# Kernel tuning notes

Measured on AMD Instinct MI355X. Metric: run time of the kernel, lower is better.

Reference implementation:

```python
import jax, jax.numpy as jnp
import numpy as np

H = 16  # n_heads (init kwarg)


def pos_enc(length, dim):
    # torch PositionalEncoding: pe[:,0::2]=sin, pe[:,1::2]=cos
    pos = jnp.arange(length, dtype=jnp.float32)[:, None]
    div = jnp.exp(jnp.arange(0, dim, 2, dtype=jnp.float32) * (-np.log(10000.0) / dim))
    ang = pos * div  # [L, dim/2]
    return jnp.stack([jnp.sin(ang), jnp.cos(ang)], axis=-1).reshape(length, dim)


def torch_ln(x, a, b, eps=1e-6):
    # custom LayerNorm: a*(x-mean)/(std+eps)+b with unbiased std (torch default)
    mean = x.mean(-1, keepdims=True)
    n = x.shape[-1]
    var = ((x - mean) ** 2).sum(-1, keepdims=True) / (n - 1)
    return a * (x - mean) / (jnp.sqrt(var) + eps) + b


def setup_inputs() -> dict:
    key = jax.random.key(0)
    ks = jax.random.split(key, 16)
    B, Lq, Lk, qd, kd, hid, mid = 8, 512, 1024, 768, 768, 1024, 4096
    s = 0.02  # weight init scale
    w = lambda k, shape: jax.random.normal(k, shape, jnp.float32) * s
    return dict(
        q=jax.random.normal(ks[0], (B, Lq, qd), jnp.float32),
        k=jax.random.normal(ks[1], (B, Lk, kd), jnp.float32),
        Wq=w(ks[2], (qd, hid)), bq=jnp.zeros(hid, jnp.float32),
        Wk=w(ks[3], (kd, hid)), bk=jnp.zeros(hid, jnp.float32),
        Wv=w(ks[4], (kd, hid)), bv=jnp.zeros(hid, jnp.float32),
        Wv0=w(ks[5], (kd, hid)), bv0=jnp.zeros(hid, jnp.float32),
        Wq0=w(ks[6], (qd, hid)), bq0=jnp.zeros(hid, jnp.float32),
        nq_a=jnp.ones(hid, jnp.float32), nq_b=jnp.zeros(hid, jnp.float32),
        nx_a=jnp.ones(hid, jnp.float32), nx_b=jnp.zeros(hid, jnp.float32),
        W1=w(ks[7], (hid, mid)), b1=jnp.zeros(mid, jnp.float32),
        W2=w(ks[8], (mid, hid)), b2=jnp.zeros(hid, jnp.float32),
        ns_a=jnp.ones(hid, jnp.float32), ns_b=jnp.zeros(hid, jnp.float32),
    )


def reference(q, k, Wq, bq, Wk, bk, Wv, bv, Wv0, bv0, Wq0, bq0,
              nq_a, nq_b, nx_a, nx_b, W1, b1, W2, b2, ns_a, ns_b):
    # FocalAtt(mode='CA').forward(q, k, PE='qk', SF=True, outmode='atted_bilinear')
    B, Lq, qd = q.shape
    Lk, kd = k.shape[1], k.shape[2]
    hid = Wq.shape[1]
    dh = hid // H
    q0 = q
    qp = q + pos_enc(Lq, qd)  # PosEnc_q (dropout=0)
    kp = k + pos_enc(Lk, kd)  # PosEnc_k
    # AttM: manual multi-head scores
    qh = (qp @ Wq + bq).reshape(B, Lq, H, dh).transpose(0, 2, 1, 3)  # bhqd
    kh = (kp @ Wk + bk).reshape(B, Lk, H, dh).transpose(0, 2, 1, 3)  # bhkd
    scores = jnp.einsum('bhqd,bhkd->bhqk', qh, kh) / jnp.sqrt(jnp.float32(dh))
    att = jax.nn.softmax(scores, axis=-1)  # SF=True
    q0p = q0 @ Wq0 + bq0  # [B, Lq, hid]
    # 'atted' branch
    v1 = (kp @ Wv + bv).reshape(B, Lk, H, dh).transpose(0, 2, 1, 3)
    atted = jnp.einsum('bhqk,bhkd->bhqd', att, v1)
    atted = atted.transpose(0, 2, 1, 3).reshape(B, Lq, hid)
    atted = torch_ln(q0p + atted, nq_a, nq_b)
    # 'bilinear' branch: einsum('bhvk,bhvq,bhqk->bhk')
    q0h = q0p.reshape(B, Lq, H, dh).transpose(0, 2, 1, 3)  # bhvd, v=Lq
    v0 = (kp @ Wv0 + bv0).reshape(B, Lk, H, dh).transpose(0, 2, 1, 3)  # bhqd, q=Lk
    x = jnp.einsum('bhvd,bhvq,bhqd->bhd', q0h, att, v0).reshape(B, hid)
    x = torch_ln(x, nx_a, nx_b)
    # attention output: relu over scores, mean over heads
    att_out = jax.nn.relu(scores).sum(axis=1) / jnp.float32(H)  # [B, Lq, Lk]
    # SorCA: FFN + residual + LayerNorm
    ff = jax.nn.relu(atted @ W1 + b1) @ W2 + b2
    qq = torch_ln(atted + ff, ns_a, ns_b)
    # FocalAtt returns (feature, q, k, attention, attidx_q, attidx_k); drop Nones
    return (x, qq, kp, att_out)
```

## Files before the change

kernel.cpp:

```cpp
#include <hip/hip_runtime.h>


typedef unsigned short bfr;
using short8 = __attribute__((ext_vector_type(8))) short;
using f32x4  = __attribute__((ext_vector_type(4))) float;

__device__ __forceinline__ float b2f(bfr s) {
  return __uint_as_float(((unsigned int)s) << 16);
}
__device__ __forceinline__ bfr f2b(float f) {
  unsigned int u = __float_as_uint(f);
  u += 0x7fffu + ((u >> 16) & 1u);
  return (bfr)(u >> 16);
}

struct __align__(8) us4 { bfr x, y, z, w; };

__device__ __forceinline__ float4 load4f(const float* p) { return *(const float4*)p; }
__device__ __forceinline__ float4 load4f(const bfr* p) {
  us4 u = *(const us4*)p;
  return make_float4(b2f(u.x), b2f(u.y), b2f(u.z), b2f(u.w));
}
__device__ __forceinline__ void store4(float* p, float a, float b, float c, float d) {
  *(float4*)p = make_float4(a, b, c, d);
}
__device__ __forceinline__ void store4(bfr* p, float a, float b, float c, float d) {
  us4 v; v.x = f2b(a); v.y = f2b(b); v.z = f2b(c); v.w = f2b(d);
  *(us4*)p = v;
}

__device__ __forceinline__ void gll16(const bfr* g, bfr* l) {
  __builtin_amdgcn_global_load_lds(
      (const __attribute__((address_space(1))) unsigned int*)g,
      (__attribute__((address_space(3))) unsigned int*)l, 16, 0, 0);
}

__device__ __forceinline__ int swz_off(int row, int chunk) {
  return row * 64 + ((chunk ^ (row & 7)) * 8);
}

__device__ __forceinline__ float pe_val(int l, int d) {
  float ang = (float)l * expf((float)(d & ~1) * (-9.210340371976184f / 768.0f));
  return (d & 1) ? cosf(ang) : sinf(ang);
}

__global__ __launch_bounds__(256) void posenc_k(const float* __restrict__ in,
                                                float* __restrict__ outf,
                                                bfr* __restrict__ outb, int total) {
  int idx = blockIdx.x * 256 + threadIdx.x;
  if (idx >= total) return;
  float v = in[idx] + pe_val((idx / 768) % 1024, idx % 768);
  outf[idx] = v;
  outb[idx] = f2b(v);
}

__global__ __launch_bounds__(256) void posenc_q_all(const float* __restrict__ in,
                                                    bfr* __restrict__ out,
                                                    bfr* __restrict__ outraw,
                                                    int total) {
  int idx = blockIdx.x * 256 + threadIdx.x;
  if (idx >= total) return;
  float v = in[idx];
  out[idx] = f2b(v + pe_val((idx / 768) % 512, idx % 768));
  outraw[idx] = f2b(v);
}

__global__ __launch_bounds__(256) void transpose_w(const float* __restrict__ src,
                                                   bfr* __restrict__ dst,
                                                   int rows, int cols, int ld,
                                                   int mode) {
  __shared__ float t[32][33];
  const int bc = blockIdx.x * 32, br = blockIdx.y * 32;
  const int tx = threadIdx.x & 31, ty = threadIdx.x >> 5;
#pragma unroll
  for (int i = 0; i < 4; i++)
    t[ty + i * 8][tx] = src[(size_t)(br + ty + i * 8) * ld + bc + tx];
  __syncthreads();
#pragma unroll
  for (int i = 0; i < 4; i++) {
    int c = bc + ty + i * 8;
    int r = (mode == 0) ? c : ((c >> 6) * 128 + (c & 63) + (mode == 2 ? 64 : 0));
    dst[(size_t)r * rows + br + tx] = f2b(t[tx][ty + i * 8]);
  }
}

template <typename TC>
__device__ __forceinline__ void mgemm_body64(const bfr* __restrict__ A,
                                             const bfr* __restrict__ BT,
                                             const float* __restrict__ bias,
                                             TC* __restrict__ C,
                                             int K, int ldc, int relu, int accum,
                                             int m0, int n0,
                                             bfr* __restrict__ As,
                                             bfr* __restrict__ Bs) {
  const int tid = threadIdx.x;
  const int lane = tid & 63, w = tid >> 6;
  const int wm = (w & 1) * 64, wn = (w >> 1) * 32;
  const int grow = lane >> 3;
  const int gkc = ((lane & 7) ^ (lane >> 3)) * 8;
  const int fr = lane & 15, fcg = lane >> 4;
  const int NT = K >> 6;
  f32x4 acc[4][2];
#pragma unroll
  for (int i = 0; i < 4; i++)
#pragma unroll
    for (int j = 0; j < 2; j++) acc[i][j] = (f32x4){0.f, 0.f, 0.f, 0.f};

  auto issue = [&](int t, int buf) {
    const int k0 = t << 6;
    const bfr* Ag = A + (size_t)(m0 + w * 32 + grow) * K + k0 + gkc;
#pragma unroll
    for (int i = 0; i < 4; i++)
      gll16(Ag + (size_t)(i * 8) * K, As + buf * 8192 + (w * 32 + i * 8) * 64);
    const bfr* Bg = BT + (size_t)(n0 + w * 16 + grow) * K + k0 + gkc;
#pragma unroll
    for (int i = 0; i < 2; i++)
      gll16(Bg + (size_t)(i * 8) * K, Bs + buf * 4096 + (w * 16 + i * 8) * 64);
  };

  issue(0, 0);
  issue(1, 1);
  asm volatile("s_waitcnt vmcnt(6)" ::: "memory");
  __builtin_amdgcn_s_barrier();
  __builtin_amdgcn_sched_barrier(0);
  int cur = 0, ib = 2;
  for (int t = 0; t < NT; ++t) {
    if (t + 2 < NT) {
      issue(t + 2, ib);
      ib = (ib == 2) ? 0 : ib + 1;
    }
    __builtin_amdgcn_s_setprio(1);
#pragma unroll
    for (int ks = 0; ks < 2; ks++) {
      short8 af[4], bf4[2];
#pragma unroll
      for (int i = 0; i < 4; i++)
        af[i] = *(const short8*)(As + cur * 8192 + swz_off(wm + i * 16 + fr, ks * 4 + fcg));
#pragma unroll
      for (int j = 0; j < 2; j++)
        bf4[j] = *(const short8*)(Bs + cur * 4096 + swz_off(wn + j * 16 + fr, ks * 4 + fcg));
#pragma unroll
      for (int i = 0; i < 4; i++)
#pragma unroll
        for (int j = 0; j < 2; j++)
          acc[i][j] = __builtin_amdgcn_mfma_f32_16x16x32_bf16(af[i], bf4[j], acc[i][j], 0, 0, 0);
    }
    __builtin_amdgcn_s_setprio(0);
    if (t + 1 < NT) {
      if (t + 2 < NT)
        asm volatile("s_waitcnt vmcnt(6)" ::: "memory");
      else
        asm volatile("s_waitcnt vmcnt(0)" ::: "memory");
      __builtin_amdgcn_s_barrier();
      __builtin_amdgcn_sched_barrier(0);
      cur = (cur == 2) ? 0 : cur + 1;
    }
  }
  const int col0 = n0 + wn + fr;
  const int row0 = m0 + wm + (lane >> 4) * 4;
  float bsv[2];
#pragma unroll
  for (int j = 0; j < 2; j++) bsv[j] = bias ? bias[col0 + j * 16] : 0.f;
#pragma unroll
  for (int i = 0; i < 4; i++) {
#pragma unroll
    for (int j = 0; j < 2; j++) {
      const int col = col0 + j * 16;
#pragma unroll
      for (int r = 0; r < 4; r++) {
        const int row = row0 + i * 16 + r;
        float v = acc[i][j][r] + bsv[j];
        if (relu) v = fmaxf(v, 0.f);
        size_t idx = (size_t)row * ldc + col;
        if constexpr (sizeof(TC) == 2) {
          C[idx] = f2b(v);
        } else {
          if (accum) C[idx] += v; else C[idx] = v;
        }
      }
    }
  }
}

template <typename TC>
__global__ __launch_bounds__(256) void mgemm64(const bfr* __restrict__ A,
                                               const bfr* __restrict__ BT,
                                               const float* __restrict__ bias,
                                               TC* __restrict__ C,
                                               int K, int ldc, int relu, int accum) {
  __shared__ bfr As[3][8192];
  __shared__ bfr Bs[3][4096];
  const int nwg = gridDim.x * gridDim.y;
  const int bid = blockIdx.y * gridDim.x + blockIdx.x;
  const int q8 = nwg >> 3, r8 = nwg & 7;
  const int xcd = bid & 7, off = bid >> 3;
  const int swz = (xcd < r8 ? xcd * (q8 + 1) : r8 * (q8 + 1) + (xcd - r8) * q8) + off;
  const int n0 = (swz % gridDim.x) * 64, m0 = (swz / gridDim.x) * 128;
  mgemm_body64<TC>(A, BT, bias, C, K, ldc, relu, accum, m0, n0,
                   &As[0][0], &Bs[0][0]);
}

__global__ __launch_bounds__(256) void kv_gemm2(const bfr* __restrict__ kp0,
                                                const bfr* __restrict__ kp1,
                                                const bfr* __restrict__ WkT,
                                                const float* __restrict__ bk,
                                                bfr* __restrict__ kh0,
                                                bfr* __restrict__ kh1,
                                                const bfr* __restrict__ WTvv,
                                                bfr* __restrict__ vT0,
                                                bfr* __restrict__ vT1) {
  __shared__ bfr As[3][8192];
  __shared__ bfr Bs[3][4096];
  const int swz = (blockIdx.x & 7) * 96 + (blockIdx.x >> 3);
  if (swz < 128) {
    mgemm_body64<bfr>(kp0, WkT, bk, kh0, 768, 1024, 0, 0,
                      (swz >> 4) * 128, (swz & 15) * 64, &As[0][0], &Bs[0][0]);
  } else if (swz < 256) {
    const int s = swz - 128;
    mgemm_body64<bfr>(kp1, WkT, bk, kh1, 768, 1024, 0, 0,
                      (s >> 4) * 128, (s & 15) * 64, &As[0][0], &Bs[0][0]);
  } else if (swz < 512) {
    const int s = swz - 256;
    mgemm_body64<bfr>(WTvv, kp0, nullptr, vT0, 768, 1024, 0, 0,
                      (s >> 4) * 128, (s & 15) * 64, &As[0][0], &Bs[0][0]);
  } else {
    const int s = swz - 512;
    mgemm_body64<bfr>(WTvv, kp1, nullptr, vT1, 768, 1024, 0, 0,
                      (s >> 4) * 128, (s & 15) * 64, &As[0][0], &Bs[0][0]);
  }
}

__global__ __launch_bounds__(256) void proj_gemm(const bfr* __restrict__ q16,
                                                 const bfr* __restrict__ Wq0T,
                                                 const float* __restrict__ bq0,
                                                 bfr* __restrict__ q0p,
                                                 const bfr* __restrict__ qp_all,
                                                 const bfr* __restrict__ WqT,
                                                 const float* __restrict__ bq,
                                                 bfr* __restrict__ qh) {
  __shared__ bfr As[3][8192];
  __shared__ bfr Bs[3][4096];
  const int swz = (blockIdx.x & 7) * 128 + (blockIdx.x >> 3);
  if (swz < 512) {
    mgemm_body64<bfr>(q16, Wq0T, bq0, q0p, 768, 1024, 0, 0,
                      (swz >> 4) * 128, (swz & 15) * 64, &As[0][0], &Bs[0][0]);
  } else {
    const int s = swz - 512;
    mgemm_body64<bfr>(qp_all, WqT, bq, qh, 768, 1024, 0, 0,
                      (s >> 4) * 128, (s & 15) * 64, &As[0][0], &Bs[0][0]);
  }
}

__global__ __launch_bounds__(256) void score_mfma(const bfr* __restrict__ qh,
                                                  const bfr* __restrict__ kh,
                                                  bfr* __restrict__ sc) {
  __shared__ __align__(16) bfr Qs[128][72];
  __shared__ __align__(16) bfr Ks[128][72];
  const int h = blockIdx.z, q0 = blockIdx.y * 128, k0 = blockIdx.x * 128;
  const int tid = threadIdx.x, lane = tid & 63;
  const int wm = ((tid >> 6) & 1) * 64, wn = (tid >> 7) * 64;
  const int fr = lane & 15, fc = (lane >> 4) * 8;
  {
    const int r = tid >> 1, c = (tid & 1) * 32;
    const bfr* qsrc = qh + (size_t)(q0 + r) * 1024 + h * 64 + c;
    const bfr* ksrc = kh + (size_t)(k0 + r) * 1024 + h * 64 + c;
#pragma unroll
    for (int i = 0; i < 4; i++) {
      *(short8*)&Qs[r][c + i * 8] = *(const short8*)(qsrc + i * 8);
      *(short8*)&Ks[r][c + i * 8] = *(const short8*)(ksrc + i * 8);
    }
  }
  __syncthreads();
  f32x4 acc[4][4];
#pragma unroll
  for (int i = 0; i < 4; i++)
#pragma unroll
    for (int j = 0; j < 4; j++) acc[i][j] = (f32x4){0.f, 0.f, 0.f, 0.f};
  __builtin_amdgcn_s_setprio(1);
#pragma unroll
  for (int ks = 0; ks < 2; ks++) {
    short8 af[4], bf[4];
#pragma unroll
    for (int t = 0; t < 4; t++) af[t] = *(const short8*)&Qs[wm + t * 16 + fr][ks * 32 + fc];
#pragma unroll
    for (int t = 0; t < 4; t++) bf[t] = *(const short8*)&Ks[wn + t * 16 + fr][ks * 32 + fc];
#pragma unroll
    for (int i = 0; i < 4; i++)
#pragma unroll
      for (int j = 0; j < 4; j++)
        acc[i][j] = __builtin_amdgcn_mfma_f32_16x16x32_bf16(af[i], bf[j], acc[i][j], 0, 0, 0);
  }
  __builtin_amdgcn_s_setprio(0);
  const int col0 = k0 + wn + fr;
  const int row0 = q0 + wm + (lane >> 4) * 4;
#pragma unroll
  for (int i = 0; i < 4; i++)
#pragma unroll
    for (int j = 0; j < 4; j++)
#pragma unroll
      for (int r = 0; r < 4; r++)
        sc[((size_t)h * 512 + row0 + i * 16 + r) * 1024 + col0 + j * 16] =
            f2b(acc[i][j][r] * 0.125f);
}

__global__ __launch_bounds__(256) void smax_ao(bfr* __restrict__ sc,
                                               float* __restrict__ ao) {
  __shared__ float part[4][1024];
  const int q = blockIdx.x;
  const int tid = threadIdx.x, lane = tid & 63, w = tid >> 6;
  float aos[16];
#pragma unroll
  for (int i = 0; i < 16; i++) aos[i] = 0.f;
#pragma unroll
  for (int i = 0; i < 4; i++) {
    const int h = w * 4 + i;
    bfr* row = sc + ((size_t)h * 512 + q) * 1024 + lane * 16;
    us4 raw[4];
    float v[16];
#pragma unroll
    for (int j = 0; j < 4; j++) raw[j] = ((const us4*)row)[j];
#pragma unroll
    for (int j = 0; j < 4; j++) {
      v[j * 4 + 0] = b2f(raw[j].x); v[j * 4 + 1] = b2f(raw[j].y);
      v[j * 4 + 2] = b2f(raw[j].z); v[j * 4 + 3] = b2f(raw[j].w);
    }
    float m = v[0];
#pragma unroll
    for (int j = 1; j < 16; j++) m = fmaxf(m, v[j]);
#pragma unroll
    for (int j = 0; j < 16; j++) aos[j] += fmaxf(v[j], 0.f);
    for (int o = 32; o; o >>= 1) m = fmaxf(m, __shfl_xor(m, o, 64));
    float s = 0.f;
#pragma unroll
    for (int j = 0; j < 16; j++) { v[j] = expf(v[j] - m); s += v[j]; }
    for (int o = 32; o; o >>= 1) s += __shfl_xor(s, o, 64);
    const float inv = 1.0f / s;
#pragma unroll
    for (int j = 0; j < 4; j++) {
      raw[j].x = f2b(v[j * 4 + 0] * inv); raw[j].y = f2b(v[j * 4 + 1] * inv);
      raw[j].z = f2b(v[j * 4 + 2] * inv); raw[j].w = f2b(v[j * 4 + 3] * inv);
      ((us4*)row)[j] = raw[j];
    }
  }
#pragma unroll
  for (int j = 0; j < 4; j++)
    *(float4*)&part[w][lane * 16 + j * 4] =
        make_float4(aos[j * 4], aos[j * 4 + 1], aos[j * 4 + 2], aos[j * 4 + 3]);
  __syncthreads();
  const int k4 = tid * 4;
  float4 a0 = *(const float4*)&part[0][k4];
  float4 a1 = *(const float4*)&part[1][k4];
  float4 a2 = *(const float4*)&part[2][k4];
  float4 a3 = *(const float4*)&part[3][k4];
  store4(ao + (size_t)q * 1024 + k4,
         (a0.x + a1.x + a2.x + a3.x) * 0.0625f, (a0.y + a1.y + a2.y + a3.y) * 0.0625f,
         (a0.z + a1.z + a2.z + a3.z) * 0.0625f, (a0.w + a1.w + a2.w + a3.w) * 0.0625f);
}

__global__ __launch_bounds__(256) void attv2(const bfr* __restrict__ att,
                                             const bfr* __restrict__ vT,
                                             const float* __restrict__ bv,
                                             const float* __restrict__ bv0,
                                             bfr* __restrict__ atp,
                                             bfr* __restrict__ u) {
  __shared__ bfr As[3][32 * 64];
  __shared__ bfr Bs[3][128 * 64];
  const int h = blockIdx.y, q0 = blockIdx.x * 32;
  const int tid = threadIdx.x, lane = tid & 63, w = tid >> 6;
  const int fr = lane & 15, fcg = lane >> 4;
  const int wm = (w & 1) * 16, wn = (w >> 1) * 64;
  const bfr* attb = att + ((size_t)h * 512 + q0) * 1024;
  const bfr* vb = vT + (size_t)h * 128 * 1024;
  const int grow = lane >> 3;
  const int gkc = ((lane & 7) ^ (lane >> 3)) * 8;
  f32x4 acc[4];
#pragma unroll
  for (int t = 0; t < 4; t++) acc[t] = (f32x4){0.f, 0.f, 0.f, 0.f};

  auto issue = [&](int t, int buf) {
    const int k0 = t << 6;
    gll16(attb + (size_t)(w * 8 + grow) * 1024 + k0 + gkc, &As[buf][(w * 8) * 64]);
#pragma unroll
    for (int i = 0; i < 4; i++)
      gll16(vb + (size_t)(w * 32 + i * 8 + grow) * 1024 + k0 + gkc,
            &Bs[buf][(w * 32 + i * 8) * 64]);
  };

  issue(0, 0);
  issue(1, 1);
  asm volatile("s_waitcnt vmcnt(5)" ::: "memory");
  __builtin_amdgcn_s_barrier();
  __builtin_amdgcn_sched_barrier(0);
  int cur = 0, ib = 2;
  for (int t = 0; t < 16; ++t) {
    if (t + 2 < 16) {
      issue(t + 2, ib);
      ib = (ib == 2) ? 0 : ib + 1;
    }
    __builtin_amdgcn_s_setprio(1);
#pragma unroll
    for (int ks = 0; ks < 2; ks++) {
      short8 af = *(const short8*)&As[cur][swz_off(wm + fr, ks * 4 + fcg)];
#pragma unroll
      for (int j = 0; j < 4; j++) {
        short8 bf = *(const short8*)&Bs[cur][swz_off(wn + j * 16 + fr, ks * 4 + fcg)];
        acc[j] = __builtin_amdgcn_mfma_f32_16x16x32_bf16(af, bf, acc[j], 0, 0, 0);
      }
    }
    __builtin_amdgcn_s_setprio(0);
    if (t + 1 < 16) {
      if (t + 2 < 16)
        asm volatile("s_waitcnt vmcnt(5)" ::: "memory");
      else
        asm volatile("s_waitcnt vmcnt(0)" ::: "memory");
      __builtin_amdgcn_s_barrier();
      __builtin_amdgcn_sched_barrier(0);
      cur = (cur == 2) ? 0 : cur + 1;
    }
  }
  const int row0 = q0 + wm + (lane >> 4) * 4;
  bfr* o = (wn == 0) ? atp : u;
  const float* bias = (wn == 0) ? bv : bv0;
#pragma unroll
  for (int t = 0; t < 4; t++) {
    const int cm = t * 16 + fr;
    const float bb = bias[h * 64 + cm];
#pragma unroll
    for (int r = 0; r < 4; r++)
      o[(size_t)(row0 + r) * 1024 + h * 64 + cm] = f2b(acc[t][r] + bb);
  }
}

__global__ __launch_bounds__(256) void xpre_kernel(const bfr* __restrict__ q0p,
                                                   const bfr* __restrict__ u,
                                                   float* __restrict__ xpre) {
  const int c = blockIdx.x * 256 + threadIdx.x;
  const int r0 = blockIdx.y * 64;
  const bfr* qp = q0p + (size_t)r0 * 1024 + c;
  const bfr* up = u + (size_t)r0 * 1024 + c;
  float s = 0.f;
#pragma unroll 8
  for (int r = 0; r < 64; r++)
    s = fmaf(b2f(qp[(size_t)r * 1024]), b2f(up[(size_t)r * 1024]), s);
  atomicAdd(&xpre[c], s);
}

template <typename TX, typename TY, typename OT>
__global__ __launch_bounds__(256) void ln_kernel(const TX* __restrict__ X,
                                                 const TY* __restrict__ Y,
                                                 const float* __restrict__ ga,
                                                 const float* __restrict__ be,
                                                 OT* __restrict__ out) {
  __shared__ float sm[4];
  const size_t row = blockIdx.x;
  const int tid = threadIdx.x;
  float4 v = load4f(X + row * 1024 + tid * 4);
  if (Y) {
    float4 w = load4f(Y + row * 1024 + tid * 4);
    v.x += w.x; v.y += w.y; v.z += w.z; v.w += w.w;
  }
  float s = v.x + v.y + v.z + v.w;
  for (int o = 32; o; o >>= 1) s += __shfl_down(s, o, 64);
  if ((tid & 63) == 0) sm[tid >> 6] = s;
  __syncthreads();
  s = sm[0] + sm[1] + sm[2] + sm[3];
  float mean = s * (1.0f / 1024.0f);
  float d0 = v.x - mean, d1 = v.y - mean, d2 = v.z - mean, d3 = v.w - mean;
  float q = d0 * d0 + d1 * d1 + d2 * d2 + d3 * d3;
  __syncthreads();
  for (int o = 32; o; o >>= 1) q += __shfl_down(q, o, 64);
  if ((tid & 63) == 0) sm[tid >> 6] = q;
  __syncthreads();
  q = sm[0] + sm[1] + sm[2] + sm[3];
  float rs = 1.0f / (sqrtf(q * (1.0f / 1023.0f)) + 1e-6f);
  float4 g = *(const float4*)(ga + tid * 4);
  float4 bb = *(const float4*)(be + tid * 4);
  store4(out + row * 1024 + tid * 4,
         g.x * d0 * rs + bb.x, g.y * d1 * rs + bb.y,
         g.z * d2 * rs + bb.z, g.w * d3 * rs + bb.w);
}

extern "C" void kernel_launch(void* const* d_in, const int* in_sizes, int n_in,
                              void* d_out, int out_size, void* d_ws, size_t ws_size,
                              hipStream_t stream) {
  (void)in_sizes; (void)n_in; (void)out_size; (void)ws_size;
  const float* q   = (const float*)d_in[0];
  const float* k   = (const float*)d_in[1];
  const float* Wq  = (const float*)d_in[2];
  const float* bq  = (const float*)d_in[3];
  const float* Wk  = (const float*)d_in[4];
  const float* bk  = (const float*)d_in[5];
  const float* Wv  = (const float*)d_in[6];
  const float* bv  = (const float*)d_in[7];
  const float* Wv0 = (const float*)d_in[8];
  const float* bv0 = (const float*)d_in[9];
  const float* Wq0 = (const float*)d_in[10];
  const float* bq0 = (const float*)d_in[11];
  const float* nqa = (const float*)d_in[12];
  const float* nqb = (const float*)d_in[13];
  const float* nxa = (const float*)d_in[14];
  const float* nxb = (const float*)d_in[15];
  const float* W1  = (const float*)d_in[16];
  const float* b1  = (const float*)d_in[17];
  const float* W2  = (const float*)d_in[18];
  const float* b2  = (const float*)d_in[19];
  const float* nsa = (const float*)d_in[20];
  const float* nsb = (const float*)d_in[21];

  float* out = (float*)d_out;
  float* x_out  = out;
  float* qq_out = out + 8192;
  float* kp_out = out + 4202496;
  float* ao_out = out + 10493952;
  bfr* kp16 = (bfr*)qq_out;
  bfr* vT1  = kp16 + 6291456;

  char* base = (char*)d_ws;
  bfr* q0p   = (bfr*)(base + 0);
  bfr* qh    = (bfr*)(base + 8388608);
  bfr* atl   = (bfr*)(base + 16777216);
  bfr* WqT   = (bfr*)(base + 25165824);
  bfr* Wq0T  = (bfr*)(base + 26738688);
  bfr* WTkv  = (bfr*)(base + 28311552);
  float* xpre = (float*)(base + 33030144);
  char* S = base + 33062912;
  bfr* sc    = (bfr*)(S + 0);
  bfr* kh0   = (bfr*)(S + 16777216);
  bfr* kh1   = (bfr*)(S + 18874368);
  bfr* vT0   = (bfr*)(S + 20971520);
  bfr* atp0  = (bfr*)(S + 16777216);
  bfr* ub0   = (bfr*)(S + 17825792);
  bfr* atp1  = (bfr*)(S + 18874368);
  bfr* ub1   = (bfr*)(S + 19922944);
  bfr* qp_all = (bfr*)(S + 0);
  bfr* q16    = (bfr*)(S + 6291456);
  bfr* W1Tn  = (bfr*)(S + 0);
  bfr* W2Tn  = (bfr*)(S + 4194304);
  bfr* ff1n  = (bfr*)(S + 8388608);
  float* ff2a = (float*)(base + 0);

  posenc_k<<<24576, 256, 0, stream>>>(k, kp_out, kp16, 6291456);
  posenc_q_all<<<12288, 256, 0, stream>>>(q, qp_all, q16, 3145728);
  transpose_w<<<dim3(32, 24), 256, 0, stream>>>(Wq, WqT, 768, 1024, 1024, 0);
  transpose_w<<<dim3(32, 24), 256, 0, stream>>>(Wq0, Wq0T, 768, 1024, 1024, 0);
  transpose_w<<<dim3(32, 24), 256, 0, stream>>>(Wk, WTkv, 768, 1024, 1024, 0);
  transpose_w<<<dim3(32, 24), 256, 0, stream>>>(Wv, WTkv + 786432, 768, 1024, 1024, 1);
  transpose_w<<<dim3(32, 24), 256, 0, stream>>>(Wv0, WTkv + 786432, 768, 1024, 1024, 2);

  proj_gemm<<<1024, 256, 0, stream>>>(q16, Wq0T, bq0, q0p, qp_all, WqT, bq, qh);
  hipMemsetAsync(xpre, 0, 32768, stream);

  for (int p = 0; p < 4; p++) {
    const int b0 = 2 * p, b1 = 2 * p + 1;
    kv_gemm2<<<768, 256, 0, stream>>>(kp16 + (size_t)b0 * 786432,
                                      kp16 + (size_t)b1 * 786432,
                                      WTkv, bk, kh0, kh1,
                                      WTkv + 786432, vT0, vT1);
    for (int j = 0; j < 2; j++) {
      const int b = b0 + j;
      bfr* kh = j ? kh1 : kh0;
      bfr* vT = j ? vT1 : vT0;
      bfr* atpb = j ? atp1 : atp0;
      bfr* ub = j ? ub1 : ub0;
      score_mfma<<<dim3(8, 4, 16), 256, 0, stream>>>(qh + (size_t)b * 524288, kh, sc);
      smax_ao<<<512, 256, 0, stream>>>(sc, ao_out + (size_t)b * 524288);
      attv2<<<dim3(16, 16), 256, 0, stream>>>(sc, vT, bv, bv0, atpb, ub);
      xpre_kernel<<<dim3(4, 8), 256, 0, stream>>>(q0p + (size_t)b * 524288, ub,
                                                  xpre + b * 1024);
      ln_kernel<bfr, bfr, bfr><<<512, 256, 0, stream>>>(
          q0p + (size_t)b * 524288, atpb, nqa, nqb, atl + (size_t)b * 524288);
    }
  }

  ln_kernel<float, float, float><<<8, 256, 0, stream>>>(xpre, (const float*)nullptr,
                                                        nxa, nxb, x_out);

  for (int nc = 0; nc < 2; nc++) {
    transpose_w<<<dim3(64, 32), 256, 0, stream>>>(W1 + nc * 2048, W1Tn,
                                                  1024, 2048, 4096, 0);
    transpose_w<<<dim3(32, 64), 256, 0, stream>>>(W2 + (size_t)nc * 2048 * 1024, W2Tn,
                                                  2048, 1024, 1024, 0);
    mgemm64<bfr><<<dim3(32, 32), 256, 0, stream>>>(
        atl, W1Tn, b1 + nc * 2048, ff1n, 1024, 2048, 1, 0);
    mgemm64<float><<<dim3(16, 32), 256, 0, stream>>>(
        ff1n, W2Tn, nc == 0 ? b2 : nullptr, ff2a, 2048, 1024, 0, nc);
  }
  ln_kernel<bfr, float, float><<<4096, 256, 0, stream>>>(atl, ff2a, nsa, nsb, qq_out);
}
```

Baseline: 780.0 us.

## Switch GEMMs to double buffering, retile attention-V, batch xpre and LayerNorm launches

```diff
diff --git a/kernel.cpp b/kernel.cpp
--- a/kernel.cpp
+++ b/kernel.cpp
@@ -119,16 +119,13 @@
   };
 
   issue(0, 0);
-  issue(1, 1);
-  asm volatile("s_waitcnt vmcnt(6)" ::: "memory");
+  asm volatile("s_waitcnt vmcnt(0)" ::: "memory");
   __builtin_amdgcn_s_barrier();
   __builtin_amdgcn_sched_barrier(0);
-  int cur = 0, ib = 2;
+  int cur = 0;
   for (int t = 0; t < NT; ++t) {
-    if (t + 2 < NT) {
-      issue(t + 2, ib);
-      ib = (ib == 2) ? 0 : ib + 1;
-    }
+    const bool more = (t + 1 < NT);
+    if (more) issue(t + 1, cur ^ 1);
     __builtin_amdgcn_s_setprio(1);
 #pragma unroll
     for (int ks = 0; ks < 2; ks++) {
@@ -146,14 +143,11 @@
           acc[i][j] = __builtin_amdgcn_mfma_f32_16x16x32_bf16(af[i], bf4[j], acc[i][j], 0, 0, 0);
     }
     __builtin_amdgcn_s_setprio(0);
-    if (t + 1 < NT) {
-      if (t + 2 < NT)
-        asm volatile("s_waitcnt vmcnt(6)" ::: "memory");
-      else
-        asm volatile("s_waitcnt vmcnt(0)" ::: "memory");
+    if (more) {
+      asm volatile("s_waitcnt vmcnt(0)" ::: "memory");
       __builtin_amdgcn_s_barrier();
       __builtin_amdgcn_sched_barrier(0);
-      cur = (cur == 2) ? 0 : cur + 1;
+      cur ^= 1;
     }
   }
   const int col0 = n0 + wn + fr;
@@ -188,8 +182,8 @@
                                                const float* __restrict__ bias,
                                                TC* __restrict__ C,
                                                int K, int ldc, int relu, int accum) {
-  __shared__ bfr As[3][8192];
-  __shared__ bfr Bs[3][4096];
+  __shared__ bfr As[2][8192];
+  __shared__ bfr Bs[2][4096];
   const int nwg = gridDim.x * gridDim.y;
   const int bid = blockIdx.y * gridDim.x + blockIdx.x;
   const int q8 = nwg >> 3, r8 = nwg & 7;
@@ -209,8 +203,8 @@
                                                 const bfr* __restrict__ WTvv,
                                                 bfr* __restrict__ vT0,
                                                 bfr* __restrict__ vT1) {
-  __shared__ bfr As[3][8192];
-  __shared__ bfr Bs[3][4096];
+  __shared__ bfr As[2][8192];
+  __shared__ bfr Bs[2][4096];
   const int swz = (blockIdx.x & 7) * 96 + (blockIdx.x >> 3);
   if (swz < 128) {
     mgemm_body64<bfr>(kp0, WkT, bk, kh0, 768, 1024, 0, 0,
@@ -238,8 +232,8 @@
                                                  const bfr* __restrict__ WqT,
                                                  const float* __restrict__ bq,
                                                  bfr* __restrict__ qh) {
-  __shared__ bfr As[3][8192];
-  __shared__ bfr Bs[3][4096];
+  __shared__ bfr As[2][8192];
+  __shared__ bfr Bs[2][4096];
   const int swz = (blockIdx.x & 7) * 128 + (blockIdx.x >> 3);
   if (swz < 512) {
     mgemm_body64<bfr>(q16, Wq0T, bq0, q0p, 768, 1024, 0, 0,
@@ -357,108 +351,94 @@
          (a0.z + a1.z + a2.z + a3.z) * 0.0625f, (a0.w + a1.w + a2.w + a3.w) * 0.0625f);
 }
 
-__global__ __launch_bounds__(256) void attv2(const bfr* __restrict__ att,
+__global__ __launch_bounds__(256) void attv3(const bfr* __restrict__ att,
                                              const bfr* __restrict__ vT,
                                              const float* __restrict__ bv,
                                              const float* __restrict__ bv0,
                                              bfr* __restrict__ atp,
                                              bfr* __restrict__ u) {
-  __shared__ bfr As[3][32 * 64];
-  __shared__ bfr Bs[3][128 * 64];
-  const int h = blockIdx.y, q0 = blockIdx.x * 32;
+  __shared__ bfr As[2][16 * 64];
+  __shared__ bfr Bs[2][128 * 64];
+  const int h = blockIdx.y, q0 = blockIdx.x * 16;
   const int tid = threadIdx.x, lane = tid & 63, w = tid >> 6;
   const int fr = lane & 15, fcg = lane >> 4;
-  const int wm = (w & 1) * 16, wn = (w >> 1) * 64;
+  const int wn = w * 32;
   const bfr* attb = att + ((size_t)h * 512 + q0) * 1024;
   const bfr* vb = vT + (size_t)h * 128 * 1024;
   const int grow = lane >> 3;
   const int gkc = ((lane & 7) ^ (lane >> 3)) * 8;
-  f32x4 acc[4];
-#pragma unroll
-  for (int t = 0; t < 4; t++) acc[t] = (f32x4){0.f, 0.f, 0.f, 0.f};
+  f32x4 acc[2];
+#pragma unroll
+  for (int j = 0; j < 2; j++) acc[j] = (f32x4){0.f, 0.f, 0.f, 0.f};
 
   auto issue = [&](int t, int buf) {
     const int k0 = t << 6;
-    gll16(attb + (size_t)(w * 8 + grow) * 1024 + k0 + gkc, &As[buf][(w * 8) * 64]);
+    if (w < 2)
+      gll16(attb + (size_t)(w * 8 + grow) * 1024 + k0 + gkc, &As[buf][(w * 8) * 64]);
 #pragma unroll
     for (int i = 0; i < 4; i++)
-      gll16(vb + (size_t)(w * 32 + i * 8 + grow) * 1024 + k0 + gkc,
-            &Bs[buf][(w * 32 + i * 8) * 64]);
+      gll16(vb + (size_t)(wn + i * 8 + grow) * 1024 + k0 + gkc,
+            &Bs[buf][(wn + i * 8) * 64]);
   };
 
   issue(0, 0);
-  issue(1, 1);
-  asm volatile("s_waitcnt vmcnt(5)" ::: "memory");
+  asm volatile("s_waitcnt vmcnt(0)" ::: "memory");
   __builtin_amdgcn_s_barrier();
   __builtin_amdgcn_sched_barrier(0);
-  int cur = 0, ib = 2;
+  int cur = 0;
   for (int t = 0; t < 16; ++t) {
-    if (t + 2 < 16) {
-      issue(t + 2, ib);
-      ib = (ib == 2) ? 0 : ib + 1;
-    }
+    const bool more = (t + 1 < 16);
+    if (more) issue(t + 1, cur ^ 1);
     __builtin_amdgcn_s_setprio(1);
 #pragma unroll
     for (int ks = 0; ks < 2; ks++) {
-      short8 af = *(const short8*)&As[cur][swz_off(wm + fr, ks * 4 + fcg)];
-#pragma unroll
-      for (int j = 0; j < 4; j++) {
+      short8 af = *(const short8*)&As[cur][swz_off(fr, ks * 4 + fcg)];
+#pragma unroll
+      for (int j = 0; j < 2; j++) {
         short8 bf = *(const short8*)&Bs[cur][swz_off(wn + j * 16 + fr, ks * 4 + fcg)];
         acc[j] = __builtin_amdgcn_mfma_f32_16x16x32_bf16(af, bf, acc[j], 0, 0, 0);
       }
     }
     __builtin_amdgcn_s_setprio(0);
-    if (t + 1 < 16) {
-      if (t + 2 < 16)
-        asm volatile("s_waitcnt vmcnt(5)" ::: "memory");
-      else
-        asm volatile("s_waitcnt vmcnt(0)" ::: "memory");
+    if (more) {
+      asm volatile("s_waitcnt vmcnt(0)" ::: "memory");
       __builtin_amdgcn_s_barrier();
       __builtin_amdgcn_sched_barrier(0);
-      cur = (cur == 2) ? 0 : cur + 1;
-    }
-  }
-  const int row0 = q0 + wm + (lane >> 4) * 4;
-  bfr* o = (wn == 0) ? atp : u;
-  const float* bias = (wn == 0) ? bv : bv0;
-#pragma unroll
-  for (int t = 0; t < 4; t++) {
-    const int cm = t * 16 + fr;
+      cur ^= 1;
+    }
+  }
+  const int row0 = q0 + (lane >> 4) * 4;
+  bfr* o = (w < 2) ? atp : u;
+  const float* bias = (w < 2) ? bv : bv0;
+  const int dbase = wn & 63;
+#pragma unroll
+  for (int j = 0; j < 2; j++) {
+    const int cm = dbase + j * 16 + fr;
     const float bb = bias[h * 64 + cm];
 #pragma unroll
     for (int r = 0; r < 4; r++)
-      o[(size_t)(row0 + r) * 1024 + h * 64 + cm] = f2b(acc[t][r] + bb);
-  }
-}
-
-__global__ __launch_bounds__(256) void xpre_kernel(const bfr* __restrict__ q0p,
-                                                   const bfr* __restrict__ u,
-                                                   float* __restrict__ xpre) {
+      o[(size_t)(row0 + r) * 1024 + h * 64 + cm] = f2b(acc[j][r] + bb);
+  }
+}
+
+__global__ __launch_bounds__(256) void xpre2(const bfr* __restrict__ q0p0,
+                                             const bfr* __restrict__ u0,
+                                             float* __restrict__ xpre0) {
   const int c = blockIdx.x * 256 + threadIdx.x;
   const int r0 = blockIdx.y * 64;
-  const bfr* qp = q0p + (size_t)r0 * 1024 + c;
-  const bfr* up = u + (size_t)r0 * 1024 + c;
+  const int j = blockIdx.z;
+  const bfr* qp = q0p0 + (size_t)j * 524288 + (size_t)r0 * 1024 + c;
+  const bfr* up = u0 + (size_t)j * 1048576 + (size_t)r0 * 1024 + c;
   float s = 0.f;
 #pragma unroll 8
   for (int r = 0; r < 64; r++)
     s = fmaf(b2f(qp[(size_t)r * 1024]), b2f(up[(size_t)r * 1024]), s);
-  atomicAdd(&xpre[c], s);
-}
-
-template <typename TX, typename TY, typename OT>
-__global__ __launch_bounds__(256) void ln_kernel(const TX* __restrict__ X,
-                                                 const TY* __restrict__ Y,
-                                                 const float* __restrict__ ga,
-                                                 const float* __restrict__ be,
-                                                 OT* __restrict__ out) {
-  __shared__ float sm[4];
-  const size_t row = blockIdx.x;
-  const int tid = threadIdx.x;
-  float4 v = load4f(X + row * 1024 + tid * 4);
-  if (Y) {
-    float4 w = load4f(Y + row * 1024 + tid * 4);
-    v.x += w.x; v.y += w.y; v.z += w.z; v.w += w.w;
-  }
+  atomicAdd(&xpre0[j * 1024 + c], s);
+}
+
+template <typename OT>
+__device__ __forceinline__ void ln_body(float4 v, const float* ga, const float* be,
+                                        OT* outp, int tid, float* sm) {
   float s = v.x + v.y + v.z + v.w;
   for (int o = 32; o; o >>= 1) s += __shfl_down(s, o, 64);
   if ((tid & 63) == 0) sm[tid >> 6] = s;
@@ -475,9 +455,40 @@
   float rs = 1.0f / (sqrtf(q * (1.0f / 1023.0f)) + 1e-6f);
   float4 g = *(const float4*)(ga + tid * 4);
   float4 bb = *(const float4*)(be + tid * 4);
-  store4(out + row * 1024 + tid * 4,
-         g.x * d0 * rs + bb.x, g.y * d1 * rs + bb.y,
+  store4(outp, g.x * d0 * rs + bb.x, g.y * d1 * rs + bb.y,
          g.z * d2 * rs + bb.z, g.w * d3 * rs + bb.w);
+}
+
+template <typename TX, typename TY, typename OT>
+__global__ __launch_bounds__(256) void ln_kernel(const TX* __restrict__ X,
+                                                 const TY* __restrict__ Y,
+                                                 const float* __restrict__ ga,
+                                                 const float* __restrict__ be,
+                                                 OT* __restrict__ out) {
+  __shared__ float sm[4];
+  const size_t row = blockIdx.x;
+  const int tid = threadIdx.x;
+  float4 v = load4f(X + row * 1024 + tid * 4);
+  if (Y) {
+    float4 w = load4f(Y + row * 1024 + tid * 4);
+    v.x += w.x; v.y += w.y; v.z += w.z; v.w += w.w;
+  }
+  ln_body(v, ga, be, out + row * 1024 + tid * 4, tid, sm);
+}
+
+__global__ __launch_bounds__(256) void ln2_kernel(const bfr* __restrict__ q0p0,
+                                                  const bfr* __restrict__ atp0,
+                                                  const float* __restrict__ ga,
+                                                  const float* __restrict__ be,
+                                                  bfr* __restrict__ atl0) {
+  __shared__ float sm[4];
+  const int row = blockIdx.x;
+  const int b = row >> 9, r = row & 511;
+  const int tid = threadIdx.x;
+  float4 v = load4f(q0p0 + (size_t)b * 524288 + (size_t)r * 1024 + tid * 4);
+  float4 w = load4f(atp0 + (size_t)b * 1048576 + (size_t)r * 1024 + tid * 4);
+  v.x += w.x; v.y += w.y; v.z += w.z; v.w += w.w;
+  ln_body(v, ga, be, atl0 + (size_t)b * 524288 + (size_t)r * 1024 + tid * 4, tid, sm);
 }
 
 extern "C" void kernel_launch(void* const* d_in, const int* in_sizes, int n_in,
@@ -551,9 +562,9 @@
   hipMemsetAsync(xpre, 0, 32768, stream);
 
   for (int p = 0; p < 4; p++) {
-    const int b0 = 2 * p, b1 = 2 * p + 1;
+    const int b0 = 2 * p;
     kv_gemm2<<<768, 256, 0, stream>>>(kp16 + (size_t)b0 * 786432,
-                                      kp16 + (size_t)b1 * 786432,
+                                      kp16 + (size_t)(b0 + 1) * 786432,
                                       WTkv, bk, kh0, kh1,
                                       WTkv + 786432, vT0, vT1);
     for (int j = 0; j < 2; j++) {
@@ -564,12 +575,12 @@
       bfr* ub = j ? ub1 : ub0;
       score_mfma<<<dim3(8, 4, 16), 256, 0, stream>>>(qh + (size_t)b * 524288, kh, sc);
       smax_ao<<<512, 256, 0, stream>>>(sc, ao_out + (size_t)b * 524288);
-      attv2<<<dim3(16, 16), 256, 0, stream>>>(sc, vT, bv, bv0, atpb, ub);
-      xpre_kernel<<<dim3(4, 8), 256, 0, stream>>>(q0p + (size_t)b * 524288, ub,
-                                                  xpre + b * 1024);
-      ln_kernel<bfr, bfr, bfr><<<512, 256, 0, stream>>>(
-          q0p + (size_t)b * 524288, atpb, nqa, nqb, atl + (size_t)b * 524288);
-    }
+      attv3<<<dim3(32, 16), 256, 0, stream>>>(sc, vT, bv, bv0, atpb, ub);
+    }
+    xpre2<<<dim3(4, 8, 2), 256, 0, stream>>>(q0p + (size_t)b0 * 524288, ub0,
+                                             xpre + b0 * 1024);
+    ln2_kernel<<<1024, 256, 0, stream>>>(q0p + (size_t)b0 * 524288, atp0,
+                                         nqa, nqb, atl + (size_t)b0 * 524288);
   }
 
   ln_kernel<float, float, float><<<8, 256, 0, stream>>>(xpre, (const float*)nullptr,
```

Measured after the change: 719.5 us. 7.8% less time.
